# Kernel optimization log

Hardware: AMD Instinct MI355X
Metric: run time of the kernel (lower is better)

The kernel has to match this reference:

```python
import jax, jax.numpy as jnp
import numpy as np

D_MODEL = 1024
H = 16
D_K = D_MODEL // H


def setup_inputs() -> dict:
    key = jax.random.key(0)
    ks = jax.random.split(key, 9)
    s = 0.02
    x = jax.random.normal(ks[0], (2, 2048, D_MODEL), dtype=jnp.float32)
    Wq = jax.random.normal(ks[1], (D_MODEL, D_MODEL), dtype=jnp.float32) * s
    bq = jax.random.normal(ks[2], (D_MODEL,), dtype=jnp.float32) * s
    Wk = jax.random.normal(ks[3], (D_MODEL, D_MODEL), dtype=jnp.float32) * s
    bk = jax.random.normal(ks[4], (D_MODEL,), dtype=jnp.float32) * s
    Wv = jax.random.normal(ks[5], (D_MODEL, D_MODEL), dtype=jnp.float32) * s
    bv = jax.random.normal(ks[6], (D_MODEL,), dtype=jnp.float32) * s
    Wo = jax.random.normal(ks[7], (D_MODEL, D_MODEL), dtype=jnp.float32) * s
    bo = jax.random.normal(ks[8], (D_MODEL,), dtype=jnp.float32) * s
    return {"x": x, "Wq": Wq, "bq": bq, "Wk": Wk, "bk": bk,
            "Wv": Wv, "bv": bv, "Wo": Wo, "bo": bo}


def reference(x, Wq, bq, Wk, bk, Wv, bv, Wo, bo):
    b, s, _ = x.shape
    scale = 1.0 / jnp.sqrt(jnp.float32(D_K))
    # projections; [b, s, d] -> [b, h, s, d_k]
    def split_heads(t):
        return t.reshape(b, s, H, D_K).transpose(0, 2, 1, 3)
    q = split_heads(x @ Wq + bq)
    k = split_heads(x @ Wk + bk)
    v = split_heads(x @ Wv + bv)
    scores = jnp.einsum('bhqd,bhkd->bhqk', q, k) * scale  # [b,h,s,s]
    attn = jax.nn.softmax(scores, axis=-1)
    ctx = jnp.einsum('bhqk,bhkd->bhqd', attn, v)
    ctx = ctx.transpose(0, 2, 1, 3).reshape(b, s, D_MODEL)
    return ctx @ Wo + bo + x
```

## Files before the change

### kernel.cpp

```cpp
#include <hip/hip_runtime.h>
#include <hip/hip_bf16.h>
#include <stdint.h>

#define D_MODEL 1024
#define NH 16
#define DK 64
#define S_LEN 2048

typedef __attribute__((ext_vector_type(8))) __bf16 bf16x8;
typedef __attribute__((ext_vector_type(4))) float f32x4;

#define GLOBAL_AS __attribute__((address_space(1)))
#define LDS_AS    __attribute__((address_space(3)))

__device__ __forceinline__ void async16(const ushort* g, ushort* l) {
    __builtin_amdgcn_global_load_lds(
        (const GLOBAL_AS uint32_t*)(uintptr_t)(const void*)g,
        (LDS_AS uint32_t*)(uint32_t)(uintptr_t)(void*)l,
        16, 0, 0);
}

__device__ __forceinline__ ushort f2bf(float f) {
    union { float f; uint32_t u; } v; v.f = f;
    uint32_t lsb = (v.u >> 16) & 1u;
    return (ushort)((v.u + 0x7fffu + lsb) >> 16);
}

__device__ __forceinline__ uint32_t packbf(float a, float b) {
    union { float f; uint32_t u; } x, y; x.f = a; y.f = b;
    return ((x.u + 0x8000u) >> 16) | ((y.u + 0x8000u) & 0xffff0000u);
}

__device__ __forceinline__ bf16x8 ldfrag(const ushort* p) {
    union { uint4 u; bf16x8 b; } cv;
    cv.u = *(const uint4*)p;
    return cv.b;
}


__global__ void cvt_x_kernel(const float* __restrict__ x, ushort* __restrict__ xb) {
    int i = blockIdx.x * 256 + threadIdx.x;
    float4 v = ((const float4*)x)[i];
    ushort4 o;
    o.x = f2bf(v.x); o.y = f2bf(v.y); o.z = f2bf(v.z); o.w = f2bf(v.w);
    ((ushort4*)xb)[i] = o;
}

__global__ void transpose_cvt4_kernel(
    const float* __restrict__ W0, const float* __restrict__ W1,
    const float* __restrict__ W2, const float* __restrict__ W3,
    ushort* __restrict__ D0, ushort* __restrict__ D1,
    ushort* __restrict__ D2, ushort* __restrict__ D3) {
    const float* W; ushort* D;
    switch (blockIdx.z) {
        case 0: W = W0; D = D0; break;
        case 1: W = W1; D = D1; break;
        case 2: W = W2; D = D2; break;
        default: W = W3; D = D3; break;
    }
    __shared__ float tile[32][33];
    int bx = blockIdx.x * 32, by = blockIdx.y * 32;
    int tx = threadIdx.x, ty = threadIdx.y;
#pragma unroll
    for (int j = 0; j < 32; j += 8)
        tile[ty + j][tx] = W[(size_t)(by + ty + j) * D_MODEL + bx + tx];
    __syncthreads();
#pragma unroll
    for (int j = 0; j < 32; j += 8)
        D[(size_t)(bx + ty + j) * D_MODEL + by + tx] = f2bf(tile[tx][ty + j]);
}

__global__ void cvt_bias_kernel(const float* __restrict__ bq, const float* __restrict__ bk,
                                const float* __restrict__ bv, float* __restrict__ out) {
    int i = blockIdx.x * 256 + threadIdx.x;
    float v = (i < 1024) ? bq[i] : (i < 2048 ? bk[i - 1024] : bv[i - 2048]);
    out[i] = v;
}

template <int MODE>
__global__ __launch_bounds__(256) void gemm_kernel(
    const ushort* __restrict__ A, const ushort* __restrict__ Bt,
    const float* __restrict__ bias,
    ushort* __restrict__ outQ, ushort* __restrict__ outK, ushort* __restrict__ outVt,
    const float* __restrict__ xres, float* __restrict__ outF) {
    __shared__ __align__(16) ushort sA[128 * 64];
    __shared__ __align__(16) ushort sB[128 * 64];
    const int tid = threadIdx.x;
    const int wave = tid >> 6, lane = tid & 63;
    const int lr = lane & 15, lq = lane >> 4;
    const int srow = lane >> 3, sp = lane & 7;
    const int blockM = blockIdx.y * 128;
    const int blockN = blockIdx.x * 128;
    const int waveM = (wave >> 1) * 64, waveN = (wave & 1) * 64;

    f32x4 acc[4][4] = {};

    for (int k0 = 0; k0 < D_MODEL; k0 += 64) {
        __syncthreads();
#pragma unroll
        for (int t = 0; t < 4; t++) {
            int row = wave * 32 + t * 8 + srow;
            int c = sp ^ (row & 7);
            async16(&A[(size_t)(blockM + row) * D_MODEL + k0 + c * 8],
                    &sA[(wave * 32 + t * 8) * 64]);
            async16(&Bt[(size_t)(blockN + row) * D_MODEL + k0 + c * 8],
                    &sB[(wave * 32 + t * 8) * 64]);
        }
        __syncthreads();
#pragma unroll
        for (int kk = 0; kk < 2; kk++) {
            bf16x8 af[4], bfr[4];
            int swz = ((kk * 4 + lq) ^ (lr & 7)) * 8;
#pragma unroll
            for (int mi = 0; mi < 4; mi++)
                af[mi] = ldfrag(&sA[(waveM + mi * 16 + lr) * 64 + swz]);
#pragma unroll
            for (int ni = 0; ni < 4; ni++)
                bfr[ni] = ldfrag(&sB[(waveN + ni * 16 + lr) * 64 + swz]);
#pragma unroll
            for (int mi = 0; mi < 4; mi++)
#pragma unroll
                for (int ni = 0; ni < 4; ni++)
                    acc[mi][ni] = __builtin_amdgcn_mfma_f32_16x16x32_bf16(
                        af[mi], bfr[ni], acc[mi][ni], 0, 0, 0);
        }
    }

#pragma unroll
    for (int mi = 0; mi < 4; mi++) {
#pragma unroll
        for (int ni = 0; ni < 4; ni++) {
#pragma unroll
            for (int r = 0; r < 4; r++) {
                int m = blockM + waveM + mi * 16 + lq * 4 + r;
                int n = blockN + waveN + ni * 16 + lr;
                float v = acc[mi][ni][r] + bias[n];
                if (MODE == 0) {
                    int which = n >> 10, c = n & 1023;
                    int h = c >> 6, d = c & 63;
                    int b = m >> 11, s = m & 2047;
                    size_t bh = (size_t)(b * NH + h);
                    if (which == 0)
                        outQ[(bh * S_LEN + s) * DK + d] = f2bf(v * 0.125f);
                    else if (which == 1)
                        outK[(bh * S_LEN + s) * DK + d] = f2bf(v);
                    else
                        outVt[(bh * DK + d) * S_LEN + s] = f2bf(v);
                } else {
                    size_t idx = (size_t)m * D_MODEL + n;
                    outF[idx] = v + xres[idx];
                }
            }
        }
    }
}

__global__ __launch_bounds__(256, 3) void attn_kernel(
    const ushort* __restrict__ Q, const ushort* __restrict__ Km,
    const ushort* __restrict__ Vt, ushort* __restrict__ ctx) {
    const int bh = blockIdx.y, qt = blockIdx.x;
    const int q0 = qt * 128;
    __shared__ __align__(16) ushort sQ[128 * 64];
    __shared__ __align__(16) ushort sK[64 * 64];
    __shared__ __align__(16) ushort sV[64 * 64];
    __shared__ __align__(16) ushort sP[4 * 32 * 72];
    const int tid = threadIdx.x;
    const int wave = tid >> 6, lane = tid & 63;
    const int lr = lane & 15, lq = lane >> 4;
    const int srow = lane >> 3, sp = lane & 7;
    const ushort* Qh = Q + (size_t)bh * S_LEN * DK;
    const ushort* Kh = Km + (size_t)bh * S_LEN * DK;
    const ushort* Vh = Vt + (size_t)bh * DK * S_LEN;
    ushort* sPw = &sP[wave * 32 * 72];

#pragma unroll
    for (int t = 0; t < 4; t++) {
        int row = wave * 32 + t * 8 + srow;
        int c = sp ^ (row & 7);
        async16(&Qh[(size_t)(q0 + row) * DK + c * 8], &sQ[(wave * 32 + t * 8) * 64]);
    }
    __syncthreads();

    bf16x8 qf[2][2];
#pragma unroll
    for (int mi = 0; mi < 2; mi++)
#pragma unroll
        for (int kk = 0; kk < 2; kk++)
            qf[mi][kk] = ldfrag(&sQ[(wave * 32 + mi * 16 + lr) * 64 +
                                    (((kk * 4 + lq) ^ (lr & 7)) * 8)]);

    f32x4 cacc[2][4] = {};
    float lsum[2] = {0.f, 0.f};

    for (int k0 = 0; k0 < S_LEN; k0 += 64) {
        __syncthreads();
#pragma unroll
        for (int t = 0; t < 2; t++) {
            int row = wave * 16 + t * 8 + srow;
            int c = sp ^ (row & 7);
            async16(&Kh[(size_t)(k0 + row) * DK + c * 8], &sK[(wave * 16 + t * 8) * 64]);
            async16(&Vh[(size_t)row * S_LEN + k0 + c * 8], &sV[(wave * 16 + t * 8) * 64]);
        }
        __syncthreads();

        f32x4 sacc[2][4] = {};
#pragma unroll
        for (int kk = 0; kk < 2; kk++) {
            bf16x8 kf[4];
            int swz = ((kk * 4 + lq) ^ (lr & 7)) * 8;
#pragma unroll
            for (int nj = 0; nj < 4; nj++)
                kf[nj] = ldfrag(&sK[(nj * 16 + lr) * 64 + swz]);
#pragma unroll
            for (int mi = 0; mi < 2; mi++)
#pragma unroll
                for (int nj = 0; nj < 4; nj++)
                    sacc[mi][nj] = __builtin_amdgcn_mfma_f32_16x16x32_bf16(
                        kf[nj], qf[mi][kk], sacc[mi][nj], 0, 0, 0);
        }

#pragma unroll
        for (int mi = 0; mi < 2; mi++) {
#pragma unroll
            for (int nj = 0; nj < 4; nj++) {
                float p0 = __expf(sacc[mi][nj][0]);
                float p1 = __expf(sacc[mi][nj][1]);
                float p2 = __expf(sacc[mi][nj][2]);
                float p3 = __expf(sacc[mi][nj][3]);
                lsum[mi] += (p0 + p1) + (p2 + p3);
                uint2 w;
                w.x = packbf(p0, p1);
                w.y = packbf(p2, p3);
                *(uint2*)&sPw[(mi * 16 + lr) * 72 + nj * 16 + lq * 4] = w;
            }
        }

#pragma unroll
        for (int ks = 0; ks < 2; ks++) {
            bf16x8 pf[2], vf[4];
#pragma unroll
            for (int mi = 0; mi < 2; mi++)
                pf[mi] = ldfrag(&sPw[(mi * 16 + lr) * 72 + ks * 32 + lq * 8]);
            int swz = ((ks * 4 + lq) ^ (lr & 7)) * 8;
#pragma unroll
            for (int nd = 0; nd < 4; nd++)
                vf[nd] = ldfrag(&sV[(nd * 16 + lr) * 64 + swz]);
#pragma unroll
            for (int mi = 0; mi < 2; mi++)
#pragma unroll
                for (int nd = 0; nd < 4; nd++)
                    cacc[mi][nd] = __builtin_amdgcn_mfma_f32_16x16x32_bf16(
                        pf[mi], vf[nd], cacc[mi][nd], 0, 0, 0);
        }
    }

    float inv[2];
#pragma unroll
    for (int mi = 0; mi < 2; mi++) {
        float l = lsum[mi];
        l += __shfl_xor(l, 16);
        l += __shfl_xor(l, 32);
        inv[mi] = 1.f / l;
    }
    float invr[2][4];
#pragma unroll
    for (int mi = 0; mi < 2; mi++)
#pragma unroll
        for (int r = 0; r < 4; r++)
            invr[mi][r] = __shfl(inv[mi], lq * 4 + r);

    const int b = bh >> 4, h = bh & 15;
#pragma unroll
    for (int mi = 0; mi < 2; mi++)
#pragma unroll
        for (int nd = 0; nd < 4; nd++)
#pragma unroll
            for (int r = 0; r < 4; r++) {
                int qrow = q0 + wave * 32 + mi * 16 + lq * 4 + r;
                int d = nd * 16 + lr;
                float v = cacc[mi][nd][r] * invr[mi][r];
                ctx[(size_t)(b * S_LEN + qrow) * D_MODEL + h * DK + d] = f2bf(v);
            }
}


extern "C" void kernel_launch(void* const* d_in, const int* in_sizes, int n_in,
                              void* d_out, int out_size, void* d_ws, size_t ws_size,
                              hipStream_t stream) {
    const float* x  = (const float*)d_in[0];
    const float* Wq = (const float*)d_in[1];
    const float* bq = (const float*)d_in[2];
    const float* Wk = (const float*)d_in[3];
    const float* bk = (const float*)d_in[4];
    const float* Wv = (const float*)d_in[5];
    const float* bv = (const float*)d_in[6];
    const float* Wo = (const float*)d_in[7];
    const float* bo = (const float*)d_in[8];

    char* ws = (char*)d_ws;
    ushort* xb    = (ushort*)(ws);
    ushort* wqkv  = (ushort*)(ws + (8ull  << 20));
    ushort* wo_t  = (ushort*)(ws + (14ull << 20));
    ushort* qbuf  = (ushort*)(ws + (16ull << 20));
    ushort* kbuf  = (ushort*)(ws + (24ull << 20));
    ushort* vtb   = (ushort*)(ws + (32ull << 20));
    ushort* ctx   = (ushort*)(ws + (40ull << 20));
    float*  biasq = (float*)(ws + (48ull << 20));

    cvt_x_kernel<<<4096, 256, 0, stream>>>(x, xb);
    transpose_cvt4_kernel<<<dim3(32, 32, 4), dim3(32, 8), 0, stream>>>(
        Wq, Wk, Wv, Wo, wqkv, wqkv + 1024 * 1024, wqkv + 2 * 1024 * 1024, wo_t);
    cvt_bias_kernel<<<12, 256, 0, stream>>>(bq, bk, bv, biasq);

    gemm_kernel<0><<<dim3(24, 32), 256, 0, stream>>>(
        xb, wqkv, biasq, qbuf, kbuf, vtb, nullptr, nullptr);
    attn_kernel<<<dim3(16, 32), 256, 0, stream>>>(qbuf, kbuf, vtb, ctx);
    gemm_kernel<1><<<dim3(8, 32), 256, 0, stream>>>(
        ctx, wo_t, bo, nullptr, nullptr, nullptr, x, (float*)d_out);
}
```

Before: 227.4 us.

## Double-buffer GEMM K-loop, shrink output GEMM tile, and remap blocks for XCD locality

The GEMM kernel now uses double-buffered 32-wide K tiles in LDS, issuing the async load of the next tile while MFMAs run on the current one. This removes the load-then-compute barrier stall of the old single-buffered loop. The output projection GEMM switches to 128x64 tiles, giving 512 blocks instead of 256 for better CU fill. GEMMs and attention now use a 1D grid with an XCD-aware block remap, so blocks sharing B columns or heads land on the same XCD and reuse its L2, at the cost of a more complex index mapping.

```diff
diff --git a/kernel.cpp b/kernel.cpp
--- a/kernel.cpp
+++ b/kernel.cpp
@@ -83,53 +83,76 @@
     const float* __restrict__ bias,
     ushort* __restrict__ outQ, ushort* __restrict__ outK, ushort* __restrict__ outVt,
     const float* __restrict__ xres, float* __restrict__ outF) {
-    __shared__ __align__(16) ushort sA[128 * 64];
-    __shared__ __align__(16) ushort sB[128 * 64];
+    constexpr int BN = (MODE == 0) ? 128 : 64;
+    constexpr int NI = (MODE == 0) ? 4 : 2;
+    __shared__ __align__(16) ushort sA[2][128 * 32];
+    __shared__ __align__(16) ushort sB[2][BN * 32];
     const int tid = threadIdx.x;
     const int wave = tid >> 6, lane = tid & 63;
     const int lr = lane & 15, lq = lane >> 4;
-    const int srow = lane >> 3, sp = lane & 7;
-    const int blockM = blockIdx.y * 128;
-    const int blockN = blockIdx.x * 128;
-    const int waveM = (wave >> 1) * 64, waveN = (wave & 1) * 64;
-
-    f32x4 acc[4][4] = {};
-
-    for (int k0 = 0; k0 < D_MODEL; k0 += 64) {
+    const int srow = lane >> 2;
+    const int sc = (lane & 3) ^ ((lane >> 4) & 3);
+
+    const int bid = blockIdx.x;
+    const int xcd = bid & 7, lb = bid >> 3;
+    int bx, by;
+    if (MODE == 0) { bx = xcd * 3 + (lb % 3); by = lb / 3; }
+    else           { bx = xcd * 2 + (lb & 1); by = lb >> 1; }
+    const int blockM = by * 128;
+    const int blockN = bx * BN;
+    const int waveM = (wave >> 1) * 64;
+    const int waveN = (MODE == 0) ? (wave & 1) * 64 : (wave & 1) * 32;
+
+    auto stage = [&](int k0, int b) {
+#pragma unroll
+        for (int t = 0; t < 2; t++) {
+            int row = wave * 32 + t * 16 + srow;
+            async16(&A[(size_t)(blockM + row) * D_MODEL + k0 + sc * 8],
+                    &sA[b][(wave * 32 + t * 16) * 32]);
+        }
+        if (MODE == 0) {
+#pragma unroll
+            for (int t = 0; t < 2; t++) {
+                int row = wave * 32 + t * 16 + srow;
+                async16(&Bt[(size_t)(blockN + row) * D_MODEL + k0 + sc * 8],
+                        &sB[b][(wave * 32 + t * 16) * 32]);
+            }
+        } else {
+            int row = wave * 16 + srow;
+            async16(&Bt[(size_t)(blockN + row) * D_MODEL + k0 + sc * 8],
+                    &sB[b][wave * 16 * 32]);
+        }
+    };
+
+    f32x4 acc[4][NI] = {};
+    const int swz = (lq ^ ((lr >> 2) & 3)) * 8;
+
+    stage(0, 0);
+    __syncthreads();
+#pragma unroll 2
+    for (int k = 0; k < 32; k++) {
+        const int cur = k & 1;
+        if (k < 31) stage((k + 1) * 32, cur ^ 1);
+        bf16x8 af[4], bfr[NI];
+#pragma unroll
+        for (int mi = 0; mi < 4; mi++)
+            af[mi] = ldfrag(&sA[cur][(waveM + mi * 16 + lr) * 32 + swz]);
+#pragma unroll
+        for (int ni = 0; ni < NI; ni++)
+            bfr[ni] = ldfrag(&sB[cur][(waveN + ni * 16 + lr) * 32 + swz]);
+#pragma unroll
+        for (int mi = 0; mi < 4; mi++)
+#pragma unroll
+            for (int ni = 0; ni < NI; ni++)
+                acc[mi][ni] = __builtin_amdgcn_mfma_f32_16x16x32_bf16(
+                    af[mi], bfr[ni], acc[mi][ni], 0, 0, 0);
         __syncthreads();
-#pragma unroll
-        for (int t = 0; t < 4; t++) {
-            int row = wave * 32 + t * 8 + srow;
-            int c = sp ^ (row & 7);
-            async16(&A[(size_t)(blockM + row) * D_MODEL + k0 + c * 8],
-                    &sA[(wave * 32 + t * 8) * 64]);
-            async16(&Bt[(size_t)(blockN + row) * D_MODEL + k0 + c * 8],
-                    &sB[(wave * 32 + t * 8) * 64]);
-        }
-        __syncthreads();
-#pragma unroll
-        for (int kk = 0; kk < 2; kk++) {
-            bf16x8 af[4], bfr[4];
-            int swz = ((kk * 4 + lq) ^ (lr & 7)) * 8;
-#pragma unroll
-            for (int mi = 0; mi < 4; mi++)
-                af[mi] = ldfrag(&sA[(waveM + mi * 16 + lr) * 64 + swz]);
-#pragma unroll
-            for (int ni = 0; ni < 4; ni++)
-                bfr[ni] = ldfrag(&sB[(waveN + ni * 16 + lr) * 64 + swz]);
-#pragma unroll
-            for (int mi = 0; mi < 4; mi++)
-#pragma unroll
-                for (int ni = 0; ni < 4; ni++)
-                    acc[mi][ni] = __builtin_amdgcn_mfma_f32_16x16x32_bf16(
-                        af[mi], bfr[ni], acc[mi][ni], 0, 0, 0);
-        }
     }
 
 #pragma unroll
     for (int mi = 0; mi < 4; mi++) {
 #pragma unroll
-        for (int ni = 0; ni < 4; ni++) {
+        for (int ni = 0; ni < NI; ni++) {
 #pragma unroll
             for (int r = 0; r < 4; r++) {
                 int m = blockM + waveM + mi * 16 + lq * 4 + r;
@@ -158,7 +181,10 @@
 __global__ __launch_bounds__(256, 3) void attn_kernel(
     const ushort* __restrict__ Q, const ushort* __restrict__ Km,
     const ushort* __restrict__ Vt, ushort* __restrict__ ctx) {
-    const int bh = blockIdx.y, qt = blockIdx.x;
+    const int bid = blockIdx.x;
+    const int xcd = bid & 7, lb = bid >> 3;
+    const int bh = xcd * 4 + (lb & 3);
+    const int qt = lb >> 2;
     const int q0 = qt * 128;
     __shared__ __align__(16) ushort sQ[128 * 64];
     __shared__ __align__(16) ushort sK[64 * 64];
@@ -312,9 +338,9 @@
         Wq, Wk, Wv, Wo, wqkv, wqkv + 1024 * 1024, wqkv + 2 * 1024 * 1024, wo_t);
     cvt_bias_kernel<<<12, 256, 0, stream>>>(bq, bk, bv, biasq);
 
-    gemm_kernel<0><<<dim3(24, 32), 256, 0, stream>>>(
+    gemm_kernel<0><<<768, 256, 0, stream>>>(
         xb, wqkv, biasq, qbuf, kbuf, vtb, nullptr, nullptr);
-    attn_kernel<<<dim3(16, 32), 256, 0, stream>>>(qbuf, kbuf, vtb, ctx);
-    gemm_kernel<1><<<dim3(8, 32), 256, 0, stream>>>(
+    attn_kernel<<<512, 256, 0, stream>>>(qbuf, kbuf, vtb, ctx);
+    gemm_kernel<1><<<512, 256, 0, stream>>>(
         ctx, wo_t, bo, nullptr, nullptr, nullptr, x, (float*)d_out);
 }
```

Result: faster. 216.5 us (-4.8%).
